# Performance work log

Measured on AMD Instinct MI355X. Metric: run time of the kernel, lower is better.

## Reference

```python
import jax, jax.numpy as jnp
import numpy as np

DIM = 2048
HEADS = 16
DIM_HEAD = 128
DIM_INNER = HEADS * DIM_HEAD
BATCH = 2
SEQ = 2048
EPS = 1e-12  # F.normalize default eps


def l2norm(t, axis=-1):
    # matches F.normalize(t, dim=axis, p=2): t / max(||t||, eps)
    n = jnp.sqrt(jnp.sum(t * t, axis=axis, keepdims=True))
    return t / jnp.maximum(n, EPS)


def setup_inputs() -> dict:
    key = jax.random.key(0)
    ks = jax.random.split(key, 5)
    x = jax.random.normal(ks[0], (BATCH, SEQ, DIM), dtype=jnp.float32)
    # NormLinear weights (torch Linear layout: [out, in]); parametrization
    # l2-normalizes rows (dim=-1) for q/k/v and columns (dim=0) for to_out.
    Wq = jax.random.normal(ks[1], (DIM_INNER, DIM), dtype=jnp.float32) / np.sqrt(DIM)
    Wk = jax.random.normal(ks[2], (DIM_INNER, DIM), dtype=jnp.float32) / np.sqrt(DIM)
    Wv = jax.random.normal(ks[3], (DIM_INNER, DIM), dtype=jnp.float32) / np.sqrt(DIM)
    Wout = jax.random.normal(ks[4], (DIM, DIM_INNER), dtype=jnp.float32) / np.sqrt(DIM_INNER)
    # Scale(dim_inner, init=1.0, scale=dim**-1): param = ones * dim**-1,
    # forward_scale = init/scale = dim, so qk_scale() starts at 1.0
    qk_scale = jnp.ones((DIM_INNER,), dtype=jnp.float32) / DIM
    return {"x": x, "Wq": Wq, "Wk": Wk, "Wv": Wv, "Wout": Wout, "qk_scale": qk_scale}


def reference(x, Wq, Wk, Wv, Wout, qk_scale):
    b, n, _ = x.shape
    # NormLinear: x @ l2norm(W, rows).T  (scale = groups**-1 = 1)
    q = jnp.einsum('bnd,ed->bne', x, l2norm(Wq, axis=-1))
    k = jnp.einsum('bnd,ed->bne', x, l2norm(Wk, axis=-1))
    v = jnp.einsum('bnd,ed->bne', x, l2norm(Wv, axis=-1))
    # split heads: b n (h d) -> b h n d
    split = lambda t: t.reshape(b, n, HEADS, DIM_HEAD).transpose(0, 2, 1, 3)
    q, k, v = split(q), split(k), split(v)
    # per-head l2norm of q and k over head dim
    q = l2norm(q, axis=-1)
    k = l2norm(k, axis=-1)
    # learned qk scale: (h d) -> h 1 d, effective = param * forward_scale(=DIM)
    q = q * (qk_scale * DIM).reshape(HEADS, 1, DIM_HEAD)
    # causal SDPA with scale = sqrt(dim_head) (unit-norm q,k in nGPT)
    attn_scale = DIM_HEAD ** 0.5
    scores = jnp.einsum('bhid,bhjd->bhij', q, k) * attn_scale
    causal = jnp.tril(jnp.ones((n, n), dtype=bool))
    scores = jnp.where(causal, scores, jnp.finfo(scores.dtype).min)
    attn = jax.nn.softmax(scores, axis=-1)
    out = jnp.einsum('bhij,bhjd->bhid', attn, v)
    # merge heads: b h n d -> b n (h d)
    out = out.transpose(0, 2, 1, 3).reshape(b, n, DIM_INNER)
    # to_out: NormLinear with norm over dim=0 of weight [DIM, DIM_INNER]
    out = jnp.einsum('bne,de->bnd', out, l2norm(Wout, axis=0))
    return out
```

## Files before the change

kernel.cpp:

```cpp
#include <hip/hip_runtime.h>


typedef __bf16 bf16x8 __attribute__((ext_vector_type(8)));
typedef float f32x4 __attribute__((ext_vector_type(4)));

__device__ __forceinline__ unsigned short f2bf(float f) {
  unsigned int u = __float_as_uint(f);
  u = u + 0x7FFFu + ((u >> 16) & 1u);
  return (unsigned short)(u >> 16);
}

__device__ __forceinline__ void async16(const void* g, void* l) {
  __builtin_amdgcn_global_load_lds(
      (const __attribute__((address_space(1))) unsigned int*)g,
      (__attribute__((address_space(3))) unsigned int*)l, 16, 0, 0);
}

#define QFOLD (2048.0f * 11.313708498984761f * 1.4426950408889634f)


__global__ __launch_bounds__(256) void prep_w_rows(
    const float* __restrict__ Wq, const float* __restrict__ Wk,
    const float* __restrict__ Wv, ushort* __restrict__ oq,
    ushort* __restrict__ ok_, ushort* __restrict__ ov) {
  const int row = blockIdx.x;
  const float* W = (blockIdx.y == 0) ? Wq : (blockIdx.y == 1) ? Wk : Wv;
  ushort* O = (blockIdx.y == 0) ? oq : (blockIdx.y == 1) ? ok_ : ov;
  const int t = threadIdx.x;
  const float4* Wr = (const float4*)(W + (size_t)row * 2048);
  float4 v0 = Wr[t];
  float4 v1 = Wr[t + 256];
  float ss = v0.x * v0.x + v0.y * v0.y + v0.z * v0.z + v0.w * v0.w +
             v1.x * v1.x + v1.y * v1.y + v1.z * v1.z + v1.w * v1.w;
  ss += __shfl_xor(ss, 1);  ss += __shfl_xor(ss, 2);
  ss += __shfl_xor(ss, 4);  ss += __shfl_xor(ss, 8);
  ss += __shfl_xor(ss, 16); ss += __shfl_xor(ss, 32);
  __shared__ float red[4];
  if ((t & 63) == 0) red[t >> 6] = ss;
  __syncthreads();
  float tot = red[0] + red[1] + red[2] + red[3];
  float sc = 1.0f / fmaxf(sqrtf(tot), 1e-12f);
  ushort4 o0, o1;
  o0.x = f2bf(v0.x * sc); o0.y = f2bf(v0.y * sc);
  o0.z = f2bf(v0.z * sc); o0.w = f2bf(v0.w * sc);
  o1.x = f2bf(v1.x * sc); o1.y = f2bf(v1.y * sc);
  o1.z = f2bf(v1.z * sc); o1.w = f2bf(v1.w * sc);
  *(ushort4*)(O + (size_t)row * 2048 + t * 4) = o0;
  *(ushort4*)(O + (size_t)row * 2048 + 1024 + t * 4) = o1;
}

__global__ __launch_bounds__(256) void wout_colss(const float* __restrict__ W,
                                                  float* __restrict__ colss) {
  const int e = blockIdx.x * 256 + threadIdx.x;
  const int d0 = blockIdx.y * 128;
  float ss = 0.f;
  #pragma unroll 8
  for (int i = 0; i < 128; ++i) {
    float v = W[(size_t)(d0 + i) * 2048 + e];
    ss += v * v;
  }
  atomicAdd(colss + e, ss);
}

__global__ __launch_bounds__(256) void wout_norm(const float* __restrict__ W,
                                                 const float* __restrict__ colss,
                                                 ushort* __restrict__ O) {
  const int idx = (blockIdx.x * 256 + threadIdx.x) * 4;
  float4 v = *(const float4*)(W + idx);
  float4 c = *(const float4*)(colss + (idx & 2047));
  ushort4 o;
  o.x = f2bf(v.x / fmaxf(sqrtf(c.x), 1e-12f));
  o.y = f2bf(v.y / fmaxf(sqrtf(c.y), 1e-12f));
  o.z = f2bf(v.z / fmaxf(sqrtf(c.z), 1e-12f));
  o.w = f2bf(v.w / fmaxf(sqrtf(c.w), 1e-12f));
  *(ushort4*)(O + idx) = o;
}

__global__ __launch_bounds__(256) void convert_x(const float* __restrict__ X,
                                                 ushort* __restrict__ O) {
  const int idx = (blockIdx.x * 256 + threadIdx.x) * 4;
  float4 v = *(const float4*)(X + idx);
  ushort4 o;
  o.x = f2bf(v.x); o.y = f2bf(v.y); o.z = f2bf(v.z); o.w = f2bf(v.w);
  *(ushort4*)(O + idx) = o;
}

__global__ __launch_bounds__(64) void qk_mhead(const float* __restrict__ qks,
                                               float* __restrict__ mh) {
  const int h = blockIdx.x, l = threadIdx.x;
  float m = fmaxf(fabsf(qks[h * 128 + l]), fabsf(qks[h * 128 + 64 + l]));
  m = fmaxf(m, __shfl_xor(m, 1));  m = fmaxf(m, __shfl_xor(m, 2));
  m = fmaxf(m, __shfl_xor(m, 4));  m = fmaxf(m, __shfl_xor(m, 8));
  m = fmaxf(m, __shfl_xor(m, 16)); m = fmaxf(m, __shfl_xor(m, 32));
  if (l == 0) mh[h] = m * QFOLD;
}

__device__ __forceinline__ void gemm_mainloop(
    const ushort* __restrict__ A, const ushort* __restrict__ Bw,
    int m0, int n0, ushort* As, ushort* Bs, f32x4 acc[4][4],
    int t, int l, int wm, int wn) {
  const int l15 = l & 15, l4 = l >> 4;
  const ushort* abase = A + (size_t)m0 * 2048;
  const ushort* bbase = Bw + (size_t)n0 * 2048;
  for (int kt = 0; kt < 32; ++kt) {
    const int k0 = kt * 64;
    __syncthreads();
    #pragma unroll
    for (int p = 0; p < 9; ++p) {
      int c = p * 256 + t;
      const ushort* src = abase;
      char* dst = (char*)As;
      int cc = c;
      if (c >= 1152) { cc = c - 1152; src = bbase; dst = (char*)Bs; }
      int r = cc / 9, dc = cc - r * 9;
      int dcc = (dc == 8) ? 0 : dc;
      async16(src + (size_t)r * 2048 + k0 + dcc * 8, dst + cc * 16);
    }
    __syncthreads();
    #pragma unroll
    for (int ks = 0; ks < 2; ++ks) {
      bf16x8 af[4], bg[4];
      #pragma unroll
      for (int f = 0; f < 4; ++f)
        af[f] = *(const bf16x8*)&As[(wm * 64 + f * 16 + l15) * 72 + ks * 32 + l4 * 8];
      #pragma unroll
      for (int f = 0; f < 4; ++f)
        bg[f] = *(const bf16x8*)&Bs[(wn * 64 + f * 16 + l15) * 72 + ks * 32 + l4 * 8];
      #pragma unroll
      for (int fm = 0; fm < 4; ++fm)
        #pragma unroll
        for (int fn = 0; fn < 4; ++fn)
          acc[fm][fn] = __builtin_amdgcn_mfma_f32_16x16x32_bf16(
              af[fm], bg[fn], acc[fm][fn], 0, 0, 0);
    }
  }
}

__global__ __launch_bounds__(256, 4) void gemm_qkv(
    const ushort* __restrict__ X, const ushort* __restrict__ Wq,
    const ushort* __restrict__ Wk, const ushort* __restrict__ Wv,
    const float* __restrict__ qks, ushort* __restrict__ qn,
    ushort* __restrict__ kn, ushort* __restrict__ vt) {
  const int z = blockIdx.z;
  const ushort* Bw = (z == 0) ? Wq : (z == 1) ? Wk : Wv;
  const int n0 = blockIdx.x * 128;
  const int m0 = blockIdx.y * 128;
  __shared__ __align__(16) ushort As[128 * 72];
  __shared__ __align__(16) ushort Bs[128 * 72];
  __shared__ float partials[2][128];
  const int t = threadIdx.x, w = t >> 6, l = t & 63;
  const int wm = w & 1, wn = w >> 1;
  const int l15 = l & 15, l4 = l >> 4;

  f32x4 acc[4][4];
  #pragma unroll
  for (int i = 0; i < 4; ++i)
    #pragma unroll
    for (int j = 0; j < 4; ++j) acc[i][j] = (f32x4){0.f, 0.f, 0.f, 0.f};

  gemm_mainloop(X, Bw, m0, n0, As, Bs, acc, t, l, wm, wn);

  const int h = n0 >> 7;
  if (z == 2) {
    #pragma unroll
    for (int fm = 0; fm < 4; ++fm) {
      int mrow = m0 + wm * 64 + fm * 16 + l4 * 4;
      int bb = mrow >> 11;
      int nn = mrow & 2047;
      #pragma unroll
      for (int fn = 0; fn < 4; ++fn) {
        int d = wn * 64 + fn * 16 + l15;
        ushort4 p;
        p.x = f2bf(acc[fm][fn][0]); p.y = f2bf(acc[fm][fn][1]);
        p.z = f2bf(acc[fm][fn][2]); p.w = f2bf(acc[fm][fn][3]);
        *(ushort4*)(vt + (size_t)((bb * 16 + h) * 128 + d) * 2048 + nn) = p;
      }
    }
  } else {
    float rs[4][4];
    #pragma unroll
    for (int fm = 0; fm < 4; ++fm)
      #pragma unroll
      for (int r = 0; r < 4; ++r) {
        float s = 0.f;
        #pragma unroll
        for (int fn = 0; fn < 4; ++fn) {
          float v = acc[fm][fn][r];
          s += v * v;
        }
        s += __shfl_xor(s, 1); s += __shfl_xor(s, 2);
        s += __shfl_xor(s, 4); s += __shfl_xor(s, 8);
        rs[fm][r] = s;
      }
    if (l15 == 0) {
      #pragma unroll
      for (int fm = 0; fm < 4; ++fm)
        #pragma unroll
        for (int r = 0; r < 4; ++r)
          partials[wn][wm * 64 + fm * 16 + l4 * 4 + r] = rs[fm][r];
    }
    __syncthreads();
    float cs[4];
    #pragma unroll
    for (int fn = 0; fn < 4; ++fn)
      cs[fn] = (z == 0) ? qks[n0 + wn * 64 + fn * 16 + l15] * QFOLD : 1.0f;
    ushort* O = (z == 0) ? qn : kn;
    #pragma unroll
    for (int fm = 0; fm < 4; ++fm)
      #pragma unroll
      for (int r = 0; r < 4; ++r) {
        int i = wm * 64 + fm * 16 + l4 * 4 + r;
        float tot = partials[0][i] + partials[1][i];
        float sc = 1.0f / fmaxf(sqrtf(tot), 1e-12f);
        #pragma unroll
        for (int fn = 0; fn < 4; ++fn)
          O[(size_t)(m0 + i) * 2048 + n0 + wn * 64 + fn * 16 + l15] =
              f2bf(acc[fm][fn][r] * sc * cs[fn]);
      }
  }
}

__global__ __launch_bounds__(256, 3) void attn_kernel(
    const ushort* __restrict__ qn, const ushort* __restrict__ kn,
    const ushort* __restrict__ vt, const float* __restrict__ mhead,
    ushort* __restrict__ ao) {
  const int hb = blockIdx.x;
  const int b = hb >> 4, h = hb & 15;
  const int qt = 31 - blockIdx.y;
  const int i0 = qt * 64;
  const int t = threadIdx.x, w = t >> 6, l = t & 63;
  const int l15 = l & 15, l4 = l >> 4;

  __shared__ __align__(16) ushort Ks[64 * 136];
  __shared__ __align__(16) ushort Vts[128 * 72];
  __shared__ __align__(16) ushort Ps[64 * 72];

  bf16x8 qf[4];
  #pragma unroll
  for (int ks = 0; ks < 4; ++ks)
    qf[ks] = *(const bf16x8*)(qn +
        (size_t)(b * 2048 + i0 + w * 16 + l15) * 2048 +
        h * 128 + ks * 32 + l4 * 8);

  f32x4 Oa[8];
  #pragma unroll
  for (int fd = 0; fd < 8; ++fd) Oa[fd] = (f32x4){0.f, 0.f, 0.f, 0.f};
  f32x4 Ol = (f32x4){0.f, 0.f, 0.f, 0.f};

  const float mh = mhead[h];
  const __bf16 one = (__bf16)1.0f;
  const bf16x8 ones = {one, one, one, one, one, one, one, one};

  const ushort* kbase = kn + (size_t)(b * 2048) * 2048 + h * 128;
  const ushort* vbase = vt + (size_t)((b * 16 + h) * 128) * 2048;

  for (int jt = 0; jt <= qt; ++jt) {
    const int j0 = jt * 64;
    __syncthreads();
    #pragma unroll
    for (int pass = 0; pass < 5; ++pass) {
      int c = pass * 256 + t;
      if (c < 1088) {
        int r = c / 17, dc = c - r * 17;
        int dcc = (dc == 16) ? 0 : dc;
        async16(kbase + (size_t)(j0 + r) * 2048 + dcc * 8, (char*)Ks + c * 16);
      }
    }
    #pragma unroll
    for (int pass = 0; pass < 5; ++pass) {
      int c = pass * 256 + t;
      if (c < 1152) {
        int r = c / 9, jc = c - r * 9;
        int jcc = (jc == 8) ? 0 : jc;
        async16(vbase + (size_t)r * 2048 + j0 + jcc * 8, (char*)Vts + c * 16);
      }
    }
    __syncthreads();

    f32x4 Sa[4];
    #pragma unroll
    for (int fj = 0; fj < 4; ++fj) {
      f32x4 s0 = (f32x4){0.f, 0.f, 0.f, 0.f};
      #pragma unroll
      for (int ks = 0; ks < 4; ++ks) {
        bf16x8 kf = *(const bf16x8*)&Ks[(fj * 16 + l15) * 136 + ks * 32 + l4 * 8];
        s0 = __builtin_amdgcn_mfma_f32_16x16x32_bf16(qf[ks], kf, s0, 0, 0, 0);
      }
      Sa[fj] = s0;
    }

    if (jt == qt) {
      #pragma unroll
      for (int fj = 0; fj < 4; ++fj)
        #pragma unroll
        for (int r = 0; r < 4; ++r) {
          int jg = fj * 16 + l15;
          int ig = w * 16 + l4 * 4 + r;
          if (jg > ig) Sa[fj][r] = -1e30f;
        }
    }

    #pragma unroll
    for (int fj = 0; fj < 4; ++fj)
      #pragma unroll
      for (int r = 0; r < 4; ++r)
        Ps[(w * 16 + l4 * 4 + r) * 72 + fj * 16 + l15] =
            f2bf(__builtin_exp2f(Sa[fj][r] - mh));

    #pragma unroll
    for (int ks = 0; ks < 2; ++ks) {
      bf16x8 p0 = *(const bf16x8*)&Ps[(w * 16 + l15) * 72 + ks * 32 + l4 * 8];
      Ol = __builtin_amdgcn_mfma_f32_16x16x32_bf16(p0, ones, Ol, 0, 0, 0);
      #pragma unroll
      for (int fd = 0; fd < 8; ++fd) {
        bf16x8 vf = *(const bf16x8*)&Vts[(fd * 16 + l15) * 72 + ks * 32 + l4 * 8];
        Oa[fd] = __builtin_amdgcn_mfma_f32_16x16x32_bf16(p0, vf, Oa[fd], 0, 0, 0);
      }
    }
  }

  #pragma unroll
  for (int r = 0; r < 4; ++r) {
    float inv = 1.0f / Ol[r];
    int ig = i0 + w * 16 + l4 * 4 + r;
    #pragma unroll
    for (int fd = 0; fd < 8; ++fd)
      ao[(size_t)(b * 2048 + ig) * 2048 + h * 128 + fd * 16 + l15] =
          f2bf(Oa[fd][r] * inv);
  }
}

__global__ __launch_bounds__(256, 4) void gemm_out(
    const ushort* __restrict__ A, const ushort* __restrict__ Bw,
    float* __restrict__ C) {
  const int n0 = blockIdx.x * 128;
  const int m0 = blockIdx.y * 128;
  __shared__ __align__(16) ushort As[128 * 72];
  __shared__ __align__(16) ushort Bs[128 * 72];
  const int t = threadIdx.x, w = t >> 6, l = t & 63;
  const int wm = w & 1, wn = w >> 1;
  const int l15 = l & 15, l4 = l >> 4;

  f32x4 acc[4][4];
  #pragma unroll
  for (int i = 0; i < 4; ++i)
    #pragma unroll
    for (int j = 0; j < 4; ++j) acc[i][j] = (f32x4){0.f, 0.f, 0.f, 0.f};

  gemm_mainloop(A, Bw, m0, n0, As, Bs, acc, t, l, wm, wn);

  #pragma unroll
  for (int fm = 0; fm < 4; ++fm)
    #pragma unroll
    for (int fn = 0; fn < 4; ++fn)
      #pragma unroll
      for (int r = 0; r < 4; ++r)
        C[(size_t)(m0 + wm * 64 + fm * 16 + l4 * 4 + r) * 2048 +
          n0 + wn * 64 + fn * 16 + l15] = acc[fm][fn][r];
}

extern "C" void kernel_launch(void* const* d_in, const int* in_sizes, int n_in,
                              void* d_out, int out_size, void* d_ws, size_t ws_size,
                              hipStream_t stream) {
  (void)in_sizes; (void)n_in; (void)out_size; (void)ws_size;
  const float* x    = (const float*)d_in[0];
  const float* Wq   = (const float*)d_in[1];
  const float* Wk   = (const float*)d_in[2];
  const float* Wv   = (const float*)d_in[3];
  const float* Wout = (const float*)d_in[4];
  const float* qks  = (const float*)d_in[5];
  char* ws = (char*)d_ws;

  ushort* wqn  = (ushort*)(ws + 0);
  ushort* wkn  = (ushort*)(ws + 8388608);
  ushort* wvn  = (ushort*)(ws + 16777216);
  ushort* wotn = (ushort*)(ws + 25165824);
  ushort* xbf  = (ushort*)(ws + 33554432);
  ushort* qn   = (ushort*)(ws + 50331648);
  ushort* kn   = (ushort*)(ws + 67108864);
  ushort* vt   = (ushort*)(ws + 83886080);
  ushort* ao   = (ushort*)(ws + 100663296);
  float* colss = (float*)(ws + 117440512);
  float* mh    = (float*)(ws + 117448704);
  float* out   = (float*)d_out;

  hipMemsetAsync(colss, 0, 2048 * sizeof(float), stream);
  prep_w_rows<<<dim3(2048, 3), 256, 0, stream>>>(Wq, Wk, Wv, wqn, wkn, wvn);
  wout_colss<<<dim3(8, 16), 256, 0, stream>>>(Wout, colss);
  wout_norm<<<4096, 256, 0, stream>>>(Wout, colss, wotn);
  convert_x<<<8192, 256, 0, stream>>>(x, xbf);
  qk_mhead<<<16, 64, 0, stream>>>(qks, mh);
  gemm_qkv<<<dim3(16, 32, 3), 256, 0, stream>>>(xbf, wqn, wkn, wvn, qks, qn, kn, vt);
  attn_kernel<<<dim3(32, 32), 256, 0, stream>>>(qn, kn, vt, mh, ao);
  gemm_out<<<dim3(16, 32), 256, 0, stream>>>(ao, wotn, out);
}
```

Before: 391.9 us.

## Double-buffer K/V loads and widen attention query tile to 128 rows

Each attention block now handles 128 query rows (two 16-row fragments per wave) instead of 64, so every K/V tile staged in shared memory is reused across twice as many queries. K/V tiles are double-buffered: the async global-to-LDS load for the next tile is issued before the current tile's MFMAs run, overlapping memory traffic with compute. Padded LDS layouts are replaced with XOR-swizzled layouts to avoid bank conflicts without extra space. The costs are more registers and LDS per block, occupancy lowered to 2 blocks per CU, and a grid of half as many blocks, which may hurt load balance across the causal triangle.

New measurement: 395.0 us. About the same (+0.8%).

```diff
diff --git a/kernel.cpp b/kernel.cpp
--- a/kernel.cpp
+++ b/kernel.cpp
@@ -220,32 +220,58 @@
   }
 }
 
-__global__ __launch_bounds__(256, 3) void attn_kernel(
+__device__ __forceinline__ void attn_stage(const ushort* kbase,
+                                           const ushort* vbase, int j0,
+                                           ushort* Kb, ushort* Vb, int t) {
+  #pragma unroll
+  for (int p = 0; p < 4; ++p) {
+    int c = p * 256 + t;
+    int j = c >> 4, ch = c & 15;
+    int g = (ch & 8) | ((ch ^ j) & 7);
+    async16(kbase + (size_t)(j0 + j) * 2048 + g * 8, (char*)Kb + c * 16);
+  }
+  #pragma unroll
+  for (int p = 0; p < 4; ++p) {
+    int c = p * 256 + t;
+    int d = c >> 3, ch = c & 7;
+    int g = (ch ^ d) & 7;
+    async16(vbase + (size_t)d * 2048 + j0 + g * 8, (char*)Vb + c * 16);
+  }
+}
+
+__global__ __launch_bounds__(256, 2) void attn_kernel(
     const ushort* __restrict__ qn, const ushort* __restrict__ kn,
     const ushort* __restrict__ vt, const float* __restrict__ mhead,
     ushort* __restrict__ ao) {
   const int hb = blockIdx.x;
   const int b = hb >> 4, h = hb & 15;
-  const int qt = 31 - blockIdx.y;
-  const int i0 = qt * 64;
+  const int y = blockIdx.y;
+  const int qt = (y < 8) ? (15 - y) : (y - 8);
+  const int i0 = qt * 128;
   const int t = threadIdx.x, w = t >> 6, l = t & 63;
   const int l15 = l & 15, l4 = l >> 4;
 
-  __shared__ __align__(16) ushort Ks[64 * 136];
-  __shared__ __align__(16) ushort Vts[128 * 72];
-  __shared__ __align__(16) ushort Ps[64 * 72];
-
-  bf16x8 qf[4];
-  #pragma unroll
-  for (int ks = 0; ks < 4; ++ks)
-    qf[ks] = *(const bf16x8*)(qn +
-        (size_t)(b * 2048 + i0 + w * 16 + l15) * 2048 +
-        h * 128 + ks * 32 + l4 * 8);
-
-  f32x4 Oa[8];
-  #pragma unroll
-  for (int fd = 0; fd < 8; ++fd) Oa[fd] = (f32x4){0.f, 0.f, 0.f, 0.f};
-  f32x4 Ol = (f32x4){0.f, 0.f, 0.f, 0.f};
+  __shared__ __align__(16) ushort Ks[2][64 * 128];
+  __shared__ __align__(16) ushort Vts[2][128 * 64];
+  __shared__ __align__(16) ushort Ps[128 * 64];
+
+  bf16x8 qf[2][4];
+  #pragma unroll
+  for (int fi = 0; fi < 2; ++fi)
+    #pragma unroll
+    for (int ks = 0; ks < 4; ++ks)
+      qf[fi][ks] = *(const bf16x8*)(qn +
+          (size_t)(b * 2048 + i0 + w * 32 + fi * 16 + l15) * 2048 +
+          h * 128 + ks * 32 + l4 * 8);
+
+  f32x4 Oa[2][8];
+  #pragma unroll
+  for (int fi = 0; fi < 2; ++fi)
+    #pragma unroll
+    for (int fd = 0; fd < 8; ++fd) Oa[fi][fd] = (f32x4){0.f, 0.f, 0.f, 0.f};
+  f32x4 Ol[2];
+  Ol[0] = (f32x4){0.f, 0.f, 0.f, 0.f};
+  Ol[1] = (f32x4){0.f, 0.f, 0.f, 0.f};
 
   const float mh = mhead[h];
   const __bf16 one = (__bf16)1.0f;
@@ -253,81 +279,86 @@
 
   const ushort* kbase = kn + (size_t)(b * 2048) * 2048 + h * 128;
   const ushort* vbase = vt + (size_t)((b * 16 + h) * 128) * 2048;
-
-  for (int jt = 0; jt <= qt; ++jt) {
+  const int jt_end = 2 * qt + 2;
+
+  attn_stage(kbase, vbase, 0, Ks[0], Vts[0], t);
+
+  for (int jt = 0; jt < jt_end; ++jt) {
+    const int buf = jt & 1;
     const int j0 = jt * 64;
     __syncthreads();
-    #pragma unroll
-    for (int pass = 0; pass < 5; ++pass) {
-      int c = pass * 256 + t;
-      if (c < 1088) {
-        int r = c / 17, dc = c - r * 17;
-        int dcc = (dc == 16) ? 0 : dc;
-        async16(kbase + (size_t)(j0 + r) * 2048 + dcc * 8, (char*)Ks + c * 16);
-      }
-    }
-    #pragma unroll
-    for (int pass = 0; pass < 5; ++pass) {
-      int c = pass * 256 + t;
-      if (c < 1152) {
-        int r = c / 9, jc = c - r * 9;
-        int jcc = (jc == 8) ? 0 : jc;
-        async16(vbase + (size_t)r * 2048 + j0 + jcc * 8, (char*)Vts + c * 16);
-      }
-    }
-    __syncthreads();
-
-    f32x4 Sa[4];
+    if (jt + 1 < jt_end)
+      attn_stage(kbase, vbase, (jt + 1) * 64, Ks[buf ^ 1], Vts[buf ^ 1], t);
+
+    f32x4 Sa[2][4];
     #pragma unroll
     for (int fj = 0; fj < 4; ++fj) {
       f32x4 s0 = (f32x4){0.f, 0.f, 0.f, 0.f};
+      f32x4 s1 = (f32x4){0.f, 0.f, 0.f, 0.f};
       #pragma unroll
       for (int ks = 0; ks < 4; ++ks) {
-        bf16x8 kf = *(const bf16x8*)&Ks[(fj * 16 + l15) * 136 + ks * 32 + l4 * 8];
-        s0 = __builtin_amdgcn_mfma_f32_16x16x32_bf16(qf[ks], kf, s0, 0, 0, 0);
-      }
-      Sa[fj] = s0;
-    }
-
-    if (jt == qt) {
-      #pragma unroll
-      for (int fj = 0; fj < 4; ++fj)
+        int g = ks * 4 + l4;
+        int phys = (g & 8) | ((g ^ l15) & 7);
+        bf16x8 kf = *(const bf16x8*)&Ks[buf][(fj * 16 + l15) * 128 + phys * 8];
+        s0 = __builtin_amdgcn_mfma_f32_16x16x32_bf16(qf[0][ks], kf, s0, 0, 0, 0);
+        s1 = __builtin_amdgcn_mfma_f32_16x16x32_bf16(qf[1][ks], kf, s1, 0, 0, 0);
+      }
+      Sa[0][fj] = s0; Sa[1][fj] = s1;
+    }
+
+    if (jt >= 2 * qt) {
+      #pragma unroll
+      for (int fi = 0; fi < 2; ++fi)
+        #pragma unroll
+        for (int fj = 0; fj < 4; ++fj)
+          #pragma unroll
+          for (int r = 0; r < 4; ++r) {
+            int jg = j0 + fj * 16 + l15;
+            int ig = i0 + w * 32 + fi * 16 + l4 * 4 + r;
+            if (jg > ig) Sa[fi][fj][r] = -1e30f;
+          }
+    }
+
+    #pragma unroll
+    for (int fi = 0; fi < 2; ++fi)
+      #pragma unroll
+      for (int fj = 0; fj < 4; ++fj) {
+        int cj = fj * 2 + (l15 >> 3);
         #pragma unroll
         for (int r = 0; r < 4; ++r) {
-          int jg = fj * 16 + l15;
-          int ig = w * 16 + l4 * 4 + r;
-          if (jg > ig) Sa[fj][r] = -1e30f;
+          int i = w * 32 + fi * 16 + l4 * 4 + r;
+          Ps[i * 64 + ((cj ^ i) & 7) * 8 + (l15 & 7)] =
+              f2bf(__builtin_exp2f(Sa[fi][fj][r] - mh));
         }
-    }
-
-    #pragma unroll
-    for (int fj = 0; fj < 4; ++fj)
-      #pragma unroll
-      for (int r = 0; r < 4; ++r)
-        Ps[(w * 16 + l4 * 4 + r) * 72 + fj * 16 + l15] =
-            f2bf(__builtin_exp2f(Sa[fj][r] - mh));
+      }
 
     #pragma unroll
     for (int ks = 0; ks < 2; ++ks) {
-      bf16x8 p0 = *(const bf16x8*)&Ps[(w * 16 + l15) * 72 + ks * 32 + l4 * 8];
-      Ol = __builtin_amdgcn_mfma_f32_16x16x32_bf16(p0, ones, Ol, 0, 0, 0);
+      int sw = ((ks * 4 + l4) ^ l15) & 7;
+      bf16x8 p0 = *(const bf16x8*)&Ps[(w * 32 + l15) * 64 + sw * 8];
+      bf16x8 p1 = *(const bf16x8*)&Ps[(w * 32 + 16 + l15) * 64 + sw * 8];
+      Ol[0] = __builtin_amdgcn_mfma_f32_16x16x32_bf16(p0, ones, Ol[0], 0, 0, 0);
+      Ol[1] = __builtin_amdgcn_mfma_f32_16x16x32_bf16(p1, ones, Ol[1], 0, 0, 0);
       #pragma unroll
       for (int fd = 0; fd < 8; ++fd) {
-        bf16x8 vf = *(const bf16x8*)&Vts[(fd * 16 + l15) * 72 + ks * 32 + l4 * 8];
-        Oa[fd] = __builtin_amdgcn_mfma_f32_16x16x32_bf16(p0, vf, Oa[fd], 0, 0, 0);
-      }
-    }
-  }
-
-  #pragma unroll
-  for (int r = 0; r < 4; ++r) {
-    float inv = 1.0f / Ol[r];
-    int ig = i0 + w * 16 + l4 * 4 + r;
-    #pragma unroll
-    for (int fd = 0; fd < 8; ++fd)
-      ao[(size_t)(b * 2048 + ig) * 2048 + h * 128 + fd * 16 + l15] =
-          f2bf(Oa[fd][r] * inv);
-  }
+        bf16x8 vf = *(const bf16x8*)&Vts[buf][(fd * 16 + l15) * 64 + sw * 8];
+        Oa[0][fd] = __builtin_amdgcn_mfma_f32_16x16x32_bf16(p0, vf, Oa[0][fd], 0, 0, 0);
+        Oa[1][fd] = __builtin_amdgcn_mfma_f32_16x16x32_bf16(p1, vf, Oa[1][fd], 0, 0, 0);
+      }
+    }
+  }
+
+  #pragma unroll
+  for (int fi = 0; fi < 2; ++fi)
+    #pragma unroll
+    for (int r = 0; r < 4; ++r) {
+      float inv = 1.0f / Ol[fi][r];
+      int ig = i0 + w * 32 + fi * 16 + l4 * 4 + r;
+      #pragma unroll
+      for (int fd = 0; fd < 8; ++fd)
+        ao[(size_t)(b * 2048 + ig) * 2048 + h * 128 + fd * 16 + l15] =
+            f2bf(Oa[fi][fd][r] * inv);
+    }
 }
 
 __global__ __launch_bounds__(256, 4) void gemm_out(
@@ -391,6 +422,6 @@
   convert_x<<<8192, 256, 0, stream>>>(x, xbf);
   qk_mhead<<<16, 64, 0, stream>>>(qks, mh);
   gemm_qkv<<<dim3(16, 32, 3), 256, 0, stream>>>(xbf, wqn, wkn, wvn, qks, qn, kn, vt);
-  attn_kernel<<<dim3(32, 32), 256, 0, stream>>>(qn, kn, vt, mh, ao);
+  attn_kernel<<<dim3(32, 16), 256, 0, stream>>>(qn, kn, vt, mh, ao);
   gemm_out<<<dim3(16, 32), 256, 0, stream>>>(ao, wotn, out);
 }
```
